# Kernel optimization log

Hardware: AMD Instinct MI355X
Metric: run time of the kernel (lower is better)

## Reference

```python
import jax, jax.numpy as jnp
import numpy as np

TOP_K = 2


def _mlp(x, w1, b1, w2, b2):
    # Linear -> GELU -> Linear (assumed MLP body)
    h = jax.nn.gelu(jnp.einsum('bsd,di->bsi', x, w1) + b1)
    return jnp.einsum('bsi,id->bsd', h, w2) + b2


def setup_inputs() -> dict:
    key = jax.random.key(0)
    ks = jax.random.split(key, 8)
    B, S, D, I, E = 2, 2048, 1024, 4096, 8
    s_in = 1.0 / np.sqrt(D)
    s_mid = 1.0 / np.sqrt(I)
    return {
        'x': jax.random.normal(ks[0], (B, S, D), jnp.float32),
        'gate_w': jax.random.normal(ks[1], (D, E), jnp.float32) * s_in,
        'gate_b': jnp.zeros((E,), jnp.float32),
        'sh_w1': jax.random.normal(ks[2], (D, I), jnp.float32) * s_in,
        'sh_b1': jnp.zeros((I,), jnp.float32),
        'sh_w2': jax.random.normal(ks[3], (I, D), jnp.float32) * s_mid,
        'sh_b2': jnp.zeros((D,), jnp.float32),
        'ew1': jax.random.normal(ks[4], (E, D, I), jnp.float32) * s_in,
        'eb1': jnp.zeros((E, I), jnp.float32),
        'ew2': jax.random.normal(ks[5], (E, I, D), jnp.float32) * s_mid,
        'eb2': jnp.zeros((E, D), jnp.float32),
    }


def reference(x, gate_w, gate_b, sh_w1, sh_b1, sh_w2, sh_b2, ew1, eb1, ew2, eb2):
    E = ew1.shape[0]
    # Router
    router_probs = jax.nn.softmax(jnp.einsum('bsd,de->bse', x, gate_w) + gate_b, axis=-1)
    expert_values, expert_indices = jax.lax.top_k(router_probs, k=TOP_K)  # (B,S,K)
    expert_values = expert_values / (jnp.sum(expert_values, axis=-1, keepdims=True) + 1e-9)
    # Dense compute of all experts (faithful to original)
    h = jax.nn.gelu(jnp.einsum('bsd,edi->bsei', x, ew1) + eb1)  # (B,S,E,I)
    all_outputs = jnp.einsum('bsei,eid->bsed', h, ew2) + eb2    # (B,S,E,D)
    # Combine: scatter top-k weights to dense (B,S,E) then weighted sum
    one_hot = jax.nn.one_hot(expert_indices, E, dtype=x.dtype)  # (B,S,K,E)
    weights_E = (one_hot * expert_values[..., None]).sum(axis=2)  # (B,S,E)
    moe_out = jnp.einsum('bse,bsed->bsd', weights_E, all_outputs)
    return x + _mlp(x, sh_w1, sh_b1, sh_w2, sh_b2) + moe_out
```

## Files before the change

### kernel.cpp

```cpp
#include <hip/hip_runtime.h>
#include <hip/hip_bf16.h>
#include <stdint.h>

typedef short bf16x8 __attribute__((ext_vector_type(8)));
typedef float f32x4  __attribute__((ext_vector_type(4)));
typedef unsigned short u16;

#define T_TOK 4096
#define D_DIM 1024
#define I_DIM 4096
#define NE    9
#define BK    32

__device__ __forceinline__ u16 f2bf(float f) {
    union { float f; uint32_t u; } v; v.f = f;
    uint32_t u = v.u;
    u += 0x7FFFu + ((u >> 16) & 1u);
    return (u16)(u >> 16);
}

__device__ __forceinline__ float gelu_fast(float v) {
    float c2 = 1.5957691216057308f * (v + 0.044715f * v * v * v);
    return v / (1.0f + __expf(-c2));
}

__device__ __forceinline__ void gl16(const void* g, void* l) {
    __builtin_amdgcn_global_load_lds(
        (const __attribute__((address_space(1))) void*)g,
        (__attribute__((address_space(3))) void*)l, 16, 0, 0);
}

#define DSR(dst, adr, IMM) \
    asm volatile("ds_read_b128 %0, %1 offset:" #IMM : "=v"(dst) : "v"(adr) : "memory")
#define WAIT_VM(N)  asm volatile("s_waitcnt vmcnt(" #N ")" ::: "memory")
#define WAIT_LGKM() asm volatile("s_waitcnt lgkmcnt(0)" ::: "memory")

__global__ void k_init(int* counts) {
    int i = threadIdx.x;
    if (i < 16) counts[i] = (i == 8) ? T_TOK : 0;
}

__global__ __launch_bounds__(256) void k_router(
    const float* __restrict__ x, const float* __restrict__ gw,
    const float* __restrict__ gb,
    int* counts, int* lists, int* tok_e, int* tok_pos, float* tok_w)
{
    int wave = threadIdx.x >> 6, lane = threadIdx.x & 63;
    int t = blockIdx.x * 4 + wave;
    const float* xr = x + (size_t)t * D_DIM;

    float a[8];
#pragma unroll
    for (int e = 0; e < 8; ++e) a[e] = 0.f;
#pragma unroll
    for (int j = 0; j < D_DIM / 64; ++j) {
        int d = lane + 64 * j;
        float xv = xr[d];
        const float4* g = (const float4*)(gw + (size_t)d * 8);
        float4 g0 = g[0], g1 = g[1];
        a[0] += xv * g0.x; a[1] += xv * g0.y; a[2] += xv * g0.z; a[3] += xv * g0.w;
        a[4] += xv * g1.x; a[5] += xv * g1.y; a[6] += xv * g1.z; a[7] += xv * g1.w;
    }
#pragma unroll
    for (int off = 32; off >= 1; off >>= 1)
#pragma unroll
        for (int e = 0; e < 8; ++e) a[e] += __shfl_xor(a[e], off);

    float l[8];
#pragma unroll
    for (int e = 0; e < 8; ++e) l[e] = a[e] + gb[e];
    float mx = l[0];
#pragma unroll
    for (int e = 1; e < 8; ++e) mx = fmaxf(mx, l[e]);
    float p[8], Z = 0.f;
#pragma unroll
    for (int e = 0; e < 8; ++e) { p[e] = expf(l[e] - mx); Z += p[e]; }
#pragma unroll
    for (int e = 0; e < 8; ++e) p[e] /= Z;

    int e0 = 0; float v0 = p[0];
#pragma unroll
    for (int e = 1; e < 8; ++e) if (p[e] > v0) { v0 = p[e]; e0 = e; }
    int e1 = -1; float v1 = -1.f;
#pragma unroll
    for (int e = 0; e < 8; ++e) if (e != e0 && p[e] > v1) { v1 = p[e]; e1 = e; }
    float denom = v0 + v1 + 1e-9f;
    float w0 = v0 / denom, w1 = v1 / denom;

    if (lane == 0) {
        int p0 = atomicAdd(&counts[e0], 1);
        int p1 = atomicAdd(&counts[e1], 1);
        lists[e0 * T_TOK + p0] = t;
        lists[e1 * T_TOK + p1] = t;
        tok_e[2 * t] = e0;  tok_e[2 * t + 1] = e1;
        tok_pos[2 * t] = p0; tok_pos[2 * t + 1] = p1;
        tok_w[2 * t] = w0;  tok_w[2 * t + 1] = w1;
    }
}

__global__ void k_prefix(const int* counts, int* offsets) {
    if (threadIdx.x == 0) {
        int o = 0;
        for (int e = 0; e < NE; ++e) { offsets[e] = o; o += counts[e]; }
        offsets[NE] = o;
    }
}

__global__ __launch_bounds__(256) void k_castx(const float* __restrict__ x,
                                               u16* __restrict__ xb)
{
    int i = (blockIdx.x * 256 + threadIdx.x) * 8;
    float4 a = *(const float4*)(x + i), b = *(const float4*)(x + i + 4);
    u16 t[8] = { f2bf(a.x), f2bf(a.y), f2bf(a.z), f2bf(a.w),
                 f2bf(b.x), f2bf(b.y), f2bf(b.z), f2bf(b.w) };
    *(bf16x8*)&xb[i] = *(bf16x8*)t;
}

__global__ __launch_bounds__(256) void k_transcast(
    const float* __restrict__ src, u16* __restrict__ dst, int K, int N)
{
    src += (size_t)blockIdx.z * K * N;
    dst += (size_t)blockIdx.z * N * K;
    __shared__ float ls[64][33];
    int t = threadIdx.x;
    int k0 = blockIdx.y * 64, n0 = blockIdx.x * 32;
    {
        int kr = t >> 2, ng = (t & 3) * 8;
        const float* s = src + (size_t)(k0 + kr) * N + n0 + ng;
        float4 v0 = *(const float4*)s, v1 = *(const float4*)(s + 4);
        ls[kr][ng + 0] = v0.x; ls[kr][ng + 1] = v0.y; ls[kr][ng + 2] = v0.z; ls[kr][ng + 3] = v0.w;
        ls[kr][ng + 4] = v1.x; ls[kr][ng + 5] = v1.y; ls[kr][ng + 6] = v1.z; ls[kr][ng + 7] = v1.w;
    }
    __syncthreads();
    int n = t >> 3, kg = (t & 7) * 8;
    u16 o[8];
#pragma unroll
    for (int j = 0; j < 8; ++j) o[j] = f2bf(ls[kg + j][n]);
    *(bf16x8*)&dst[(size_t)(n0 + n) * K + k0 + kg] = *(bf16x8*)o;
}

template <int GEMM>
__global__ __launch_bounds__(256, 4)
void k_gemm(const u16* __restrict__ A, const u16* __restrict__ Bt,
            const float* __restrict__ be, const float* __restrict__ bsh,
            const int* __restrict__ counts, const int* __restrict__ offsets,
            const int* __restrict__ lists, void* __restrict__ Cg)
{
    constexpr int K  = (GEMM == 1) ? D_DIM : I_DIM;
    constexpr int N  = (GEMM == 1) ? I_DIM : D_DIM;
    constexpr int NT = N / 128;
    constexpr int nk = K / BK;

    const int bid = blockIdx.x;
    const int g  = ((bid >> 3) >> 5) * 8 + (bid & 7);
    const int mt = (bid >> 3) & 31;
    const int e  = g / NT, nt = g % NT;
    const int cnt = counts[e];
    if (mt * 128 >= cnt) return;
    const int off = offsets[e];

    __shared__ __align__(16) u16 As0[4096], As1[4096], Bs0[4096], Bs1[4096];

    const int tid = threadIdx.x, w = tid >> 6, l = tid & 63;
    const int wu = __builtin_amdgcn_readfirstlane(w);
    const int wr = w >> 1, wc = w & 1;

    const int scol = ((l & 3) ^ ((l >> 3) & 3)) * 8;
    const uint32_t rch  = (uint32_t)(((l >> 4) ^ (((l & 15) >> 1) & 3)) << 4);
    const uint32_t aoff = (uint32_t)((wr * 64 + (l & 15)) * 64) + rch;
    const uint32_t boff = (uint32_t)((wc * 64 + (l & 15)) * 64) + rch;
    const uint32_t adr_a0 = (uint32_t)(uintptr_t)As0 + aoff;
    const uint32_t adr_a1 = (uint32_t)(uintptr_t)As1 + aoff;
    const uint32_t adr_b0 = (uint32_t)(uintptr_t)Bs0 + boff;
    const uint32_t adr_b1 = (uint32_t)(uintptr_t)Bs1 + boff;

    const u16* Be = Bt + (size_t)e * N * K;
    const u16* aptr[2];
    const u16* bptr[2];
#pragma unroll
    for (int q = 0; q < 2; ++q) {
        int row = mt * 128 + w * 32 + q * 16 + (l >> 2);
        int srow;
        if constexpr (GEMM == 1) {
            if (e == 8) srow = row;
            else        srow = lists[e * T_TOK + (row < cnt ? row : cnt - 1)];
        } else {
            srow = off + row;
        }
        aptr[q] = A + (size_t)srow * K + scol;
        bptr[q] = Be + (size_t)(nt * 128 + w * 32 + q * 16 + (l >> 2)) * K + scol;
    }

    f32x4 zero = {0.f, 0.f, 0.f, 0.f};
    f32x4 acc[4][4];
#pragma unroll
    for (int m = 0; m < 4; ++m)
#pragma unroll
        for (int n = 0; n < 4; ++n) acc[m][n] = zero;

    auto STG = [&](u16* Asb, u16* Bsb, int kt) {
        const int ko = kt * BK;
#pragma unroll
        for (int q = 0; q < 2; ++q) {
            gl16(aptr[q] + ko, Asb + wu * 1024 + q * 512);
            gl16(bptr[q] + ko, Bsb + wu * 1024 + q * 512);
        }
    };
    auto RDM = [&](uint32_t aA, uint32_t aB, bool st, u16* sA, u16* sB, int knext) {
        bf16x8 fa[4], fb[4];
        DSR(fa[0], aA, 0);    DSR(fa[1], aA, 1024);
        DSR(fa[2], aA, 2048); DSR(fa[3], aA, 3072);
        DSR(fb[0], aB, 0);    DSR(fb[1], aB, 1024);
        DSR(fb[2], aB, 2048); DSR(fb[3], aB, 3072);
        WAIT_LGKM();
        __builtin_amdgcn_sched_barrier(0);
        __builtin_amdgcn_s_barrier();
        if (st) STG(sA, sB, knext);
        __builtin_amdgcn_s_setprio(1);
#pragma unroll
        for (int m = 0; m < 4; ++m)
#pragma unroll
            for (int n = 0; n < 4; ++n)
                acc[m][n] = __builtin_amdgcn_mfma_f32_16x16x32_bf16(fa[m], fb[n], acc[m][n], 0, 0, 0);
        __builtin_amdgcn_s_setprio(0);
    };

    STG(As0, Bs0, 0);
    STG(As1, Bs1, 1);
    for (int kt = 0; kt < nk - 2; kt += 2) {
        WAIT_VM(4);
        __builtin_amdgcn_s_barrier();
        RDM(adr_a0, adr_b0, true, As0, Bs0, kt + 2);
        WAIT_VM(4);
        __builtin_amdgcn_s_barrier();
        RDM(adr_a1, adr_b1, true, As1, Bs1, kt + 3);
    }
    WAIT_VM(4);
    __builtin_amdgcn_s_barrier();
    RDM(adr_a0, adr_b0, false, As0, Bs0, 0);
    WAIT_VM(0);
    __builtin_amdgcn_s_barrier();
    RDM(adr_a1, adr_b1, false, As1, Bs1, 0);

    const float* bias = (e == 8) ? bsh : (be + (size_t)e * N);
#pragma unroll
    for (int m = 0; m < 4; ++m) {
        int pbase = mt * 128 + wr * 64 + m * 16 + (l >> 4) * 4;
#pragma unroll
        for (int n = 0; n < 4; ++n) {
            int gcol = nt * 128 + wc * 64 + n * 16 + (l & 15);
            float bv = bias[gcol];
#pragma unroll
            for (int r = 0; r < 4; ++r) {
                int pos = pbase + r;
                if (pos < cnt) {
                    float v = acc[m][n][r] + bv;
                    if constexpr (GEMM == 1)
                        ((u16*)Cg)[(size_t)(off + pos) * N + gcol] = f2bf(gelu_fast(v));
                    else
                        ((float*)Cg)[(size_t)(off + pos) * N + gcol] = v;
                }
            }
        }
    }
}

__global__ __launch_bounds__(256) void k_combine(
    const float* __restrict__ x, const float* __restrict__ P,
    const int* __restrict__ offsets, const int* __restrict__ tok_e,
    const int* __restrict__ tok_pos, const float* __restrict__ tok_w,
    float* __restrict__ out)
{
    int t = blockIdx.x;
    int e0 = tok_e[2 * t], e1 = tok_e[2 * t + 1];
    int r0 = offsets[e0] + tok_pos[2 * t];
    int r1 = offsets[e1] + tok_pos[2 * t + 1];
    int rs = offsets[8] + t;
    float w0 = tok_w[2 * t], w1 = tok_w[2 * t + 1];
    int i = threadIdx.x * 4;

    float4 xv = *(const float4*)(x + (size_t)t * D_DIM + i);
    float4 ps = *(const float4*)(P + (size_t)rs * D_DIM + i);
    float4 p0 = *(const float4*)(P + (size_t)r0 * D_DIM + i);
    float4 p1 = *(const float4*)(P + (size_t)r1 * D_DIM + i);
    float4 o;
    o.x = xv.x + ps.x + w0 * p0.x + w1 * p1.x;
    o.y = xv.y + ps.y + w0 * p0.y + w1 * p1.y;
    o.z = xv.z + ps.z + w0 * p0.z + w1 * p1.z;
    o.w = xv.w + ps.w + w0 * p0.w + w1 * p1.w;
    *(float4*)(out + (size_t)t * D_DIM + i) = o;
}

extern "C" void kernel_launch(void* const* d_in, const int* in_sizes, int n_in,
                              void* d_out, int out_size, void* d_ws, size_t ws_size,
                              hipStream_t stream)
{
    const float* x   = (const float*)d_in[0];
    const float* gw  = (const float*)d_in[1];
    const float* gb  = (const float*)d_in[2];
    const float* sw1 = (const float*)d_in[3];
    const float* sb1 = (const float*)d_in[4];
    const float* sw2 = (const float*)d_in[5];
    const float* sb2 = (const float*)d_in[6];
    const float* ew1 = (const float*)d_in[7];
    const float* eb1 = (const float*)d_in[8];
    const float* ew2 = (const float*)d_in[9];
    const float* eb2 = (const float*)d_in[10];

    char* w = (char*)d_ws;
    int* counts  = (int*)w;
    int* offsets = (int*)(w + 64);
    int* tok_e   = (int*)(w + 2048);
    int* tok_pos = tok_e + 2 * T_TOK;
    float* tok_w = (float*)(tok_pos + 2 * T_TOK);
    int* lists   = (int*)(tok_w + 2 * T_TOK);

    size_t o = (size_t)1 << 20;
    u16* xb  = (u16*)(w + o);
    o += (size_t)T_TOK * D_DIM * 2;
    u16* H   = (u16*)(w + o);
    o += (size_t)3 * T_TOK * I_DIM * 2;
    u16* Wt  = (u16*)(w + o);
    o += (size_t)NE * I_DIM * D_DIM * 2;
    float* P = (float*)(w + o);

    k_init<<<1, 64, 0, stream>>>(counts);

    k_transcast<<<dim3(I_DIM / 32, D_DIM / 64, 8), 256, 0, stream>>>(ew1, Wt, D_DIM, I_DIM);
    k_transcast<<<dim3(I_DIM / 32, D_DIM / 64, 1), 256, 0, stream>>>(
        sw1, Wt + (size_t)8 * I_DIM * D_DIM, D_DIM, I_DIM);
    k_castx<<<T_TOK * D_DIM / (256 * 8), 256, 0, stream>>>(x, xb);

    k_router<<<T_TOK / 4, 256, 0, stream>>>(x, gw, gb, counts, lists, tok_e, tok_pos, tok_w);
    k_prefix<<<1, 64, 0, stream>>>(counts, offsets);

    k_gemm<1><<<NE * (I_DIM / 128) * 32, 256, 0, stream>>>(
        xb, Wt, eb1, sb1, counts, offsets, lists, (void*)H);

    k_transcast<<<dim3(D_DIM / 32, I_DIM / 64, 8), 256, 0, stream>>>(ew2, Wt, I_DIM, D_DIM);
    k_transcast<<<dim3(D_DIM / 32, I_DIM / 64, 1), 256, 0, stream>>>(
        sw2, Wt + (size_t)8 * I_DIM * D_DIM, I_DIM, D_DIM);

    k_gemm<2><<<NE * (D_DIM / 128) * 32, 256, 0, stream>>>(
        H, Wt, eb2, sb2, counts, offsets, lists, (void*)P);

    k_combine<<<T_TOK, 256, 0, stream>>>(x, P, offsets, tok_e, tok_pos, tok_w, (float*)d_out);
}
```

Measured before the change: 577.7 us.

## Widen GEMM tiles to 128x256 with eight waves per block

Changes the grouped expert GEMM from 128x128 tiles with 4 waves to 128x256 tiles with 8 waves. Each block now loads one A chunk and two B chunks per K step into a doubled B shared buffer, so each A tile is reused across twice as many output columns. The aim is to cut global and LDS traffic for A and raise arithmetic intensity. In exchange there are fewer blocks and 2 blocks per CU instead of 4, plus more shared memory per block; the grid is padded so that group indices at or above the real count exit early.

Result: slower. 632.7 us (+9.5%).

```diff
diff --git a/kernel.cpp b/kernel.cpp
--- a/kernel.cpp
+++ b/kernel.cpp
@@ -140,32 +140,36 @@
 }
 
 template <int GEMM>
-__global__ __launch_bounds__(256, 4)
+__global__ __launch_bounds__(512, 2)
 void k_gemm(const u16* __restrict__ A, const u16* __restrict__ Bt,
             const float* __restrict__ be, const float* __restrict__ bsh,
             const int* __restrict__ counts, const int* __restrict__ offsets,
             const int* __restrict__ lists, void* __restrict__ Cg)
 {
-    constexpr int K  = (GEMM == 1) ? D_DIM : I_DIM;
-    constexpr int N  = (GEMM == 1) ? I_DIM : D_DIM;
-    constexpr int NT = N / 128;
-    constexpr int nk = K / BK;
+    constexpr int K   = (GEMM == 1) ? D_DIM : I_DIM;
+    constexpr int N   = (GEMM == 1) ? I_DIM : D_DIM;
+    constexpr int NT2 = N / 256;
+    constexpr int G   = NE * NT2;
+    constexpr int nk  = K / BK;
 
     const int bid = blockIdx.x;
-    const int g  = ((bid >> 3) >> 5) * 8 + (bid & 7);
-    const int mt = (bid >> 3) & 31;
-    const int e  = g / NT, nt = g % NT;
+    const int gi  = ((bid >> 3) >> 5) * 8 + (bid & 7);
+    const int mt  = (bid >> 3) & 31;
+    if (gi >= G) return;
+    const int e = gi / NT2, nt = gi % NT2;
     const int cnt = counts[e];
     if (mt * 128 >= cnt) return;
     const int off = offsets[e];
 
-    __shared__ __align__(16) u16 As0[4096], As1[4096], Bs0[4096], Bs1[4096];
+    __shared__ __align__(16) u16 As0[4096], As1[4096];
+    __shared__ __align__(16) u16 Bs0[8192], Bs1[8192];
 
     const int tid = threadIdx.x, w = tid >> 6, l = tid & 63;
     const int wu = __builtin_amdgcn_readfirstlane(w);
-    const int wr = w >> 1, wc = w & 1;
+    const int wr = w >> 2, wc = w & 3;
 
     const int scol = ((l & 3) ^ ((l >> 3) & 3)) * 8;
+    const int srow = w * 16 + (l >> 2);
     const uint32_t rch  = (uint32_t)(((l >> 4) ^ (((l & 15) >> 1) & 3)) << 4);
     const uint32_t aoff = (uint32_t)((wr * 64 + (l & 15)) * 64) + rch;
     const uint32_t boff = (uint32_t)((wc * 64 + (l & 15)) * 64) + rch;
@@ -175,20 +179,21 @@
     const uint32_t adr_b1 = (uint32_t)(uintptr_t)Bs1 + boff;
 
     const u16* Be = Bt + (size_t)e * N * K;
-    const u16* aptr[2];
+    const u16* aptr;
     const u16* bptr[2];
-#pragma unroll
-    for (int q = 0; q < 2; ++q) {
-        int row = mt * 128 + w * 32 + q * 16 + (l >> 2);
-        int srow;
+    {
+        int row = mt * 128 + srow;
+        int sr;
         if constexpr (GEMM == 1) {
-            if (e == 8) srow = row;
-            else        srow = lists[e * T_TOK + (row < cnt ? row : cnt - 1)];
+            if (e == 8) sr = row;
+            else        sr = lists[e * T_TOK + (row < cnt ? row : cnt - 1)];
         } else {
-            srow = off + row;
+            sr = off + row;
         }
-        aptr[q] = A + (size_t)srow * K + scol;
-        bptr[q] = Be + (size_t)(nt * 128 + w * 32 + q * 16 + (l >> 2)) * K + scol;
+        aptr = A + (size_t)sr * K + scol;
+#pragma unroll
+        for (int j = 0; j < 2; ++j)
+            bptr[j] = Be + (size_t)(nt * 256 + j * 128 + srow) * K + scol;
     }
 
     f32x4 zero = {0.f, 0.f, 0.f, 0.f};
@@ -200,11 +205,10 @@
 
     auto STG = [&](u16* Asb, u16* Bsb, int kt) {
         const int ko = kt * BK;
-#pragma unroll
-        for (int q = 0; q < 2; ++q) {
-            gl16(aptr[q] + ko, Asb + wu * 1024 + q * 512);
-            gl16(bptr[q] + ko, Bsb + wu * 1024 + q * 512);
-        }
+        gl16(aptr + ko, Asb + wu * 512);
+#pragma unroll
+        for (int j = 0; j < 2; ++j)
+            gl16(bptr[j] + ko, Bsb + j * 4096 + wu * 512);
     };
     auto RDM = [&](uint32_t aA, uint32_t aB, bool st, u16* sA, u16* sB, int knext) {
         bf16x8 fa[4], fb[4];
@@ -228,14 +232,14 @@
     STG(As0, Bs0, 0);
     STG(As1, Bs1, 1);
     for (int kt = 0; kt < nk - 2; kt += 2) {
-        WAIT_VM(4);
+        WAIT_VM(3);
         __builtin_amdgcn_s_barrier();
         RDM(adr_a0, adr_b0, true, As0, Bs0, kt + 2);
-        WAIT_VM(4);
+        WAIT_VM(3);
         __builtin_amdgcn_s_barrier();
         RDM(adr_a1, adr_b1, true, As1, Bs1, kt + 3);
     }
-    WAIT_VM(4);
+    WAIT_VM(3);
     __builtin_amdgcn_s_barrier();
     RDM(adr_a0, adr_b0, false, As0, Bs0, 0);
     WAIT_VM(0);
@@ -248,7 +252,7 @@
         int pbase = mt * 128 + wr * 64 + m * 16 + (l >> 4) * 4;
 #pragma unroll
         for (int n = 0; n < 4; ++n) {
-            int gcol = nt * 128 + wc * 64 + n * 16 + (l & 15);
+            int gcol = nt * 256 + wc * 64 + n * 16 + (l & 15);
             float bv = bias[gcol];
 #pragma unroll
             for (int r = 0; r < 4; ++r) {
@@ -334,14 +338,14 @@
     k_router<<<T_TOK / 4, 256, 0, stream>>>(x, gw, gb, counts, lists, tok_e, tok_pos, tok_w);
     k_prefix<<<1, 64, 0, stream>>>(counts, offsets);
 
-    k_gemm<1><<<NE * (I_DIM / 128) * 32, 256, 0, stream>>>(
+    k_gemm<1><<<144 * 32, 512, 0, stream>>>(
         xb, Wt, eb1, sb1, counts, offsets, lists, (void*)H);
 
     k_transcast<<<dim3(D_DIM / 32, I_DIM / 64, 8), 256, 0, stream>>>(ew2, Wt, I_DIM, D_DIM);
     k_transcast<<<dim3(D_DIM / 32, I_DIM / 64, 1), 256, 0, stream>>>(
         sw2, Wt + (size_t)8 * I_DIM * D_DIM, I_DIM, D_DIM);
 
-    k_gemm<2><<<NE * (D_DIM / 128) * 32, 256, 0, stream>>>(
+    k_gemm<2><<<40 * 32, 512, 0, stream>>>(
         H, Wt, eb2, sb2, counts, offsets, lists, (void*)P);
 
     k_combine<<<T_TOK, 256, 0, stream>>>(x, P, offsets, tok_e, tok_pos, tok_w, (float*)d_out);
```

## Triple-buffer GEMM LDS pipeline and fuse x bf16 cast into router

Applied to the files above, without the earlier changes.

The GEMM main loop goes from a two-stage to a three-stage LDS ring buffer, so two tiles are in flight while one is computed, with the waits and tail steps adjusted to match. Launch bounds drop to 3 waves per SIMD to make room for the extra 16 KB of shared memory. Separately, the standalone bf16 cast kernel for x is removed and the cast is done inside the router, which already reads x. The router writes bf16 scalar-by-scalar rather than in vectors, and the lower occupancy could cost latency hiding.

Measured after the change: 573.7 us. About the same (-0.7%).

```diff
diff --git a/kernel.cpp b/kernel.cpp
--- a/kernel.cpp
+++ b/kernel.cpp
@@ -32,8 +32,8 @@
 
 #define DSR(dst, adr, IMM) \
     asm volatile("ds_read_b128 %0, %1 offset:" #IMM : "=v"(dst) : "v"(adr) : "memory")
-#define WAIT_VM(N)  asm volatile("s_waitcnt vmcnt(" #N ")" ::: "memory")
-#define WAIT_LGKM() asm volatile("s_waitcnt lgkmcnt(0)" ::: "memory")
+#define WAIT_VM(N)   asm volatile("s_waitcnt vmcnt(" #N ")" ::: "memory")
+#define WAIT_LG(N)   asm volatile("s_waitcnt lgkmcnt(" #N ")" ::: "memory")
 
 __global__ void k_init(int* counts) {
     int i = threadIdx.x;
@@ -43,11 +43,13 @@
 __global__ __launch_bounds__(256) void k_router(
     const float* __restrict__ x, const float* __restrict__ gw,
     const float* __restrict__ gb,
-    int* counts, int* lists, int* tok_e, int* tok_pos, float* tok_w)
+    int* counts, int* lists, int* tok_e, int* tok_pos, float* tok_w,
+    u16* __restrict__ xb)
 {
     int wave = threadIdx.x >> 6, lane = threadIdx.x & 63;
     int t = blockIdx.x * 4 + wave;
     const float* xr = x + (size_t)t * D_DIM;
+    u16* xbr = xb + (size_t)t * D_DIM;
 
     float a[8];
 #pragma unroll
@@ -56,6 +58,7 @@
     for (int j = 0; j < D_DIM / 64; ++j) {
         int d = lane + 64 * j;
         float xv = xr[d];
+        xbr[d] = f2bf(xv);
         const float4* g = (const float4*)(gw + (size_t)d * 8);
         float4 g0 = g[0], g1 = g[1];
         a[0] += xv * g0.x; a[1] += xv * g0.y; a[2] += xv * g0.z; a[3] += xv * g0.w;
@@ -104,16 +107,6 @@
         for (int e = 0; e < NE; ++e) { offsets[e] = o; o += counts[e]; }
         offsets[NE] = o;
     }
-}
-
-__global__ __launch_bounds__(256) void k_castx(const float* __restrict__ x,
-                                               u16* __restrict__ xb)
-{
-    int i = (blockIdx.x * 256 + threadIdx.x) * 8;
-    float4 a = *(const float4*)(x + i), b = *(const float4*)(x + i + 4);
-    u16 t[8] = { f2bf(a.x), f2bf(a.y), f2bf(a.z), f2bf(a.w),
-                 f2bf(b.x), f2bf(b.y), f2bf(b.z), f2bf(b.w) };
-    *(bf16x8*)&xb[i] = *(bf16x8*)t;
 }
 
 __global__ __launch_bounds__(256) void k_transcast(
@@ -140,7 +133,7 @@
 }
 
 template <int GEMM>
-__global__ __launch_bounds__(256, 4)
+__global__ __launch_bounds__(256, 3)
 void k_gemm(const u16* __restrict__ A, const u16* __restrict__ Bt,
             const float* __restrict__ be, const float* __restrict__ bsh,
             const int* __restrict__ counts, const int* __restrict__ offsets,
@@ -159,7 +152,8 @@
     if (mt * 128 >= cnt) return;
     const int off = offsets[e];
 
-    __shared__ __align__(16) u16 As0[4096], As1[4096], Bs0[4096], Bs1[4096];
+    __shared__ __align__(16) u16 As0[4096], As1[4096], As2[4096];
+    __shared__ __align__(16) u16 Bs0[4096], Bs1[4096], Bs2[4096];
 
     const int tid = threadIdx.x, w = tid >> 6, l = tid & 63;
     const int wu = __builtin_amdgcn_readfirstlane(w);
@@ -171,8 +165,10 @@
     const uint32_t boff = (uint32_t)((wc * 64 + (l & 15)) * 64) + rch;
     const uint32_t adr_a0 = (uint32_t)(uintptr_t)As0 + aoff;
     const uint32_t adr_a1 = (uint32_t)(uintptr_t)As1 + aoff;
+    const uint32_t adr_a2 = (uint32_t)(uintptr_t)As2 + aoff;
     const uint32_t adr_b0 = (uint32_t)(uintptr_t)Bs0 + boff;
     const uint32_t adr_b1 = (uint32_t)(uintptr_t)Bs1 + boff;
+    const uint32_t adr_b2 = (uint32_t)(uintptr_t)Bs2 + boff;
 
     const u16* Be = Bt + (size_t)e * N * K;
     const u16* aptr[2];
@@ -212,7 +208,7 @@
         DSR(fa[2], aA, 2048); DSR(fa[3], aA, 3072);
         DSR(fb[0], aB, 0);    DSR(fb[1], aB, 1024);
         DSR(fb[2], aB, 2048); DSR(fb[3], aB, 3072);
-        WAIT_LGKM();
+        WAIT_LG(0);
         __builtin_amdgcn_sched_barrier(0);
         __builtin_amdgcn_s_barrier();
         if (st) STG(sA, sB, knext);
@@ -227,19 +223,24 @@
 
     STG(As0, Bs0, 0);
     STG(As1, Bs1, 1);
-    for (int kt = 0; kt < nk - 2; kt += 2) {
-        WAIT_VM(4);
-        __builtin_amdgcn_s_barrier();
-        RDM(adr_a0, adr_b0, true, As0, Bs0, kt + 2);
-        WAIT_VM(4);
-        __builtin_amdgcn_s_barrier();
-        RDM(adr_a1, adr_b1, true, As1, Bs1, kt + 3);
-    }
-    WAIT_VM(4);
-    __builtin_amdgcn_s_barrier();
+    STG(As2, Bs2, 2);
+    for (int b = 0; b + 5 < nk; b += 3) {
+        WAIT_VM(8); __builtin_amdgcn_s_barrier();
+        RDM(adr_a0, adr_b0, true, As0, Bs0, b + 3);
+        WAIT_VM(8); __builtin_amdgcn_s_barrier();
+        RDM(adr_a1, adr_b1, true, As1, Bs1, b + 4);
+        WAIT_VM(8); __builtin_amdgcn_s_barrier();
+        RDM(adr_a2, adr_b2, true, As2, Bs2, b + 5);
+    }
+    WAIT_VM(8); __builtin_amdgcn_s_barrier();
+    RDM(adr_a0, adr_b0, true, As0, Bs0, nk - 2);
+    WAIT_VM(8); __builtin_amdgcn_s_barrier();
+    RDM(adr_a1, adr_b1, true, As1, Bs1, nk - 1);
+    WAIT_VM(8); __builtin_amdgcn_s_barrier();
+    RDM(adr_a2, adr_b2, false, As2, Bs2, 0);
+    WAIT_VM(4); __builtin_amdgcn_s_barrier();
     RDM(adr_a0, adr_b0, false, As0, Bs0, 0);
-    WAIT_VM(0);
-    __builtin_amdgcn_s_barrier();
+    WAIT_VM(0); __builtin_amdgcn_s_barrier();
     RDM(adr_a1, adr_b1, false, As1, Bs1, 0);
 
     const float* bias = (e == 8) ? bsh : (be + (size_t)e * N);
@@ -329,9 +330,8 @@
     k_transcast<<<dim3(I_DIM / 32, D_DIM / 64, 8), 256, 0, stream>>>(ew1, Wt, D_DIM, I_DIM);
     k_transcast<<<dim3(I_DIM / 32, D_DIM / 64, 1), 256, 0, stream>>>(
         sw1, Wt + (size_t)8 * I_DIM * D_DIM, D_DIM, I_DIM);
-    k_castx<<<T_TOK * D_DIM / (256 * 8), 256, 0, stream>>>(x, xb);
-
-    k_router<<<T_TOK / 4, 256, 0, stream>>>(x, gw, gb, counts, lists, tok_e, tok_pos, tok_w);
+
+    k_router<<<T_TOK / 4, 256, 0, stream>>>(x, gw, gb, counts, lists, tok_e, tok_pos, tok_w, xb);
     k_prefix<<<1, 64, 0, stream>>>(counts, offsets);
 
     k_gemm<1><<<NE * (I_DIM / 128) * 32, 256, 0, stream>>>(
```
